# Performance work log

Hardware: AMD Instinct MI355X
Metric: run time of the kernel (lower is better)

The kernel has to match this reference:

```python
import jax
jax.config.update("jax_enable_x64", True)
import jax.numpy as jnp
import numpy as np

# NTT-friendly stand-in prime for BLS12-377 Fr (residues fit in int64, products in 62 bits)
P = 2013265921          # 15 * 2^27 + 1
GEN = 31                # generator of (Z/P)^*
COSET = 7               # coset shift generator
LOG_DOMAIN = 21
DOMAIN = 1 << LOG_DOMAIN
BATCH = 8


def _pow_table(base, length):
    """numpy int64 table [base^0, ..., base^(length-1)] mod P, built by doubling."""
    t = np.ones(length, dtype=np.int64)
    k = 1
    while k < length:
        mult = pow(int(base), k, P)          # exact python-int exponentiation
        end = min(2 * k, length)
        t[k:end] = (t[:end - k] * mult) % P  # < 2^62, no overflow
        k = end
    return t


def _bitrev(n):
    b = int(n).bit_length() - 1
    idx = np.arange(n, dtype=np.int64)
    rev = np.zeros(n, dtype=np.int64)
    for i in range(b):
        rev |= ((idx >> i) & 1) << (b - 1 - i)
    return rev


def _ntt_core(x, inverse):
    """Iterative radix-2 Cooley-Tukey NTT over rows of x: [batch, n] int64 residues mod P."""
    b, n = x.shape
    logn = n.bit_length() - 1
    root = pow(GEN, (P - 1) // n, P)         # primitive n-th root of unity
    if inverse:
        root = pow(root, P - 2, P)
    wpow = _pow_table(root, n // 2)          # root^j, j < n/2 (host-side, exact)
    x = x[:, jnp.asarray(_bitrev(n))]        # bit-reversal permutation
    for s in range(1, logn + 1):             # structural loop over log2(n) stages
        m = 1 << s
        half = m >> 1
        tw = jnp.asarray(wpow[:: n // m][:half])   # stage twiddles root^{j*n/m}
        xr = x.reshape(b, n // m, m)
        e, o = xr[..., :half], xr[..., half:]
        t = (o * tw) % P                     # butterfly: vectorized over all groups
        x = jnp.concatenate([(e + t) % P, (e - t) % P], axis=-1).reshape(b, n)
    return x


def setup_inputs() -> dict:
    key = jax.random.key(0)
    inp = jax.random.randint(key, (BATCH, DOMAIN), 0, P, dtype=jnp.int64)
    return {"input": inp, "is_intt": 0, "is_coset": 0}


def reference(input, is_intt, is_coset):
    x = jnp.mod(input, P)
    n = x.shape[-1]
    if (not is_intt) and is_coset:
        # coset NTT: multiply element i by COSET^i before the forward transform
        x = (x * jnp.asarray(_pow_table(COSET, n))) % P
    x = _ntt_core(x, inverse=bool(is_intt))
    if is_intt:
        if is_coset:
            # coset INTT: undo the coset shift after the inverse transform
            x = (x * jnp.asarray(_pow_table(pow(COSET, P - 2, P), n))) % P
        n_inv = pow(int(n), P - 2, P)
        x = (x * n_inv) % P                  # scale by n^{-1}
    return x
```

## Files before the change

kernel.cpp:

```cpp
#include <hip/hip_runtime.h>
#include <stdint.h>

typedef unsigned int u32;
typedef unsigned long long u64;

#define MOD_P 2013265921u

#define T_A      0
#define T_B      16384
#define T_W128P  32768
#define T_RP     49152
#define T_CLP    49216
#define T_CHP    65600
#define T_NINV   65728

__device__ __forceinline__ u32 mul64mod(u32 a, u32 b){ return (u32)((u64)a * b % MOD_P); }

__device__ u32 powmod(u32 b, u32 e){
  u32 r = 1;
  while (e){ if (e & 1) r = mul64mod(r, b); b = mul64mod(b, b); e >>= 1; }
  return r;
}

__device__ __forceinline__ u32 shoup_of(u32 v){ return (u32)(((u64)v << 32) / MOD_P); }

__device__ __forceinline__ u32 redP(u32 a){
  u32 b = a - MOD_P;
  return b < a ? b : a;
}

__device__ __forceinline__ u32 mul_shoup(u32 a, uint2 t){
  u32 q = __umulhi(a, t.y);
  u32 r = a * t.x - q * MOD_P;
  return redP(r);
}

__device__ __forceinline__ constexpr int rev4(int m){
  return ((m&1)<<3) | ((m&2)<<1) | ((m&4)>>1) | ((m&8)>>3);
}

__device__ __forceinline__ void bf(u32 &x, u32 &y, uint2 t){
  u32 s = redP(x + y);
  u32 d = x - y + MOD_P;
  x = s; y = mul_shoup(d, t);
}
__device__ __forceinline__ void bf0(u32 &x, u32 &y){
  u32 s = redP(x + y);
  u32 d = x - y + MOD_P;
  x = s; y = d;
}

__device__ __forceinline__ void stages_p1(u32 v[16], int b, const uint2* __restrict__ twl){
  #pragma unroll
  for (int m = 0; m < 8; ++m) bf(v[m], v[m+8], twl[b + 8*m]);
  #pragma unroll
  for (int g = 0; g < 2; ++g)
    #pragma unroll
    for (int m = 0; m < 4; ++m) bf(v[g*8+m], v[g*8+m+4], twl[(b + 8*m) << 1]);
  #pragma unroll
  for (int g = 0; g < 4; ++g)
    #pragma unroll
    for (int m = 0; m < 2; ++m) bf(v[g*4+m], v[g*4+m+2], twl[(b + 8*m) << 2]);
  #pragma unroll
  for (int k = 0; k < 8; ++k) bf(v[2*k], v[2*k+1], twl[b << 3]);
}
__device__ __forceinline__ void stages_p2(u32 v[16], const uint2* __restrict__ twl){
  #pragma unroll
  for (int g = 0; g < 2; ++g)
    #pragma unroll
    for (int m = 0; m < 4; ++m) bf(v[g*8+m], v[g*8+m+4], twl[m << 4]);
  #pragma unroll
  for (int g = 0; g < 4; ++g)
    #pragma unroll
    for (int m = 0; m < 2; ++m) bf(v[g*4+m], v[g*4+m+2], twl[m << 5]);
  #pragma unroll
  for (int k = 0; k < 8; ++k) bf0(v[2*k], v[2*k+1]);
}

__device__ __forceinline__ int cidx(int row, int a){
  return (row << 7) | (a ^ (row >> 2));
}

extern "C" __global__ void k_gen(uint2* __restrict__ tw, const int* __restrict__ f_intt){
  const u32 tid = blockIdx.x * 256 + threadIdx.x;
  const int intt = f_intt[0];
  const u32 MASK = (1u << 21) - 1;
  u32 v; int dst;
  if (tid < 16384){
    u32 e = (tid >> 7) * (tid & 127);
    if (intt) e = ((1u<<21) - e) & MASK;
    v = powmod(31u, 960u * e); dst = T_A + tid;
  } else if (tid < 32768){
    u32 i = tid - 16384;
    u32 e = (((i >> 7) * (i & 127)) << 7) & MASK;
    if (intt) e = ((1u<<21) - e) & MASK;
    v = powmod(31u, 960u * e); dst = T_B + i;
  } else if (tid < 49152){
    u32 i = tid - 32768;
    u32 e = (i << 7) & MASK;
    if (intt) e = ((1u<<21) - e) & MASK;
    v = powmod(31u, 960u * e); dst = T_W128P + i;
  } else if (tid < 65536){
    u32 i = tid - 49152;
    v = intt ? powmod(7u, (MOD_P - 1 - i) % (MOD_P - 1)) : powmod(7u, i);
    dst = T_CLP + i;
  } else if (tid < 65664){
    u32 e = (tid - 65536) << 14;
    v = intt ? powmod(7u, MOD_P - 1 - e) : powmod(7u, e);
    dst = T_CHP + (tid - 65536);
  } else if (tid < 65728){
    u32 e = ((tid - 65664) << 14) & MASK;
    if (intt) e = ((1u<<21) - e) & MASK;
    v = powmod(31u, 960u * e); dst = T_RP + (tid - 65664);
  } else if (tid == 65728){
    v = powmod(1u << 21, MOD_P - 2); dst = T_NINV;
  } else return;
  tw[dst] = make_uint2(v, shoup_of(v));
}

extern "C" __global__ void __launch_bounds__(1024, 8) k_passA_z(
    const u32* __restrict__ x, u32* __restrict__ z, const uint2* __restrict__ tw,
    const int* __restrict__ f_intt, const int* __restrict__ f_coset)
{
  __shared__ u32 lds[16384];
  const int wg = blockIdx.x;
  const int jb = wg & 127;
  const int batch = wg >> 7;
  const int t = threadIdx.x;
  const u32* xb = x + ((size_t)batch << 21) + (jb << 7);
  u32* zb = z + ((size_t)batch << 21) + (jb << 14);
  const uint2* twl = tw + T_RP;
  {
    const int q = t & 31, rr = t >> 5;
    uint4 tmp[4];
    #pragma unroll
    for (int i = 0; i < 4; ++i)
      tmp[i] = *(const uint4*)(xb + ((size_t)(rr + 32*i) << 14) + (q << 2));
    #pragma unroll
    for (int i = 0; i < 4; ++i){
      u32* d = &lds[((rr + 32*i) << 7) | (q << 2)];
      d[0] = redP(tmp[i].x); d[1] = redP(tmp[i].y);
      d[2] = redP(tmp[i].z); d[3] = redP(tmp[i].w);
    }
  }
  __syncthreads();
  const int jc = t & 127;
  const int b = __builtin_amdgcn_readfirstlane(t >> 7);
  u32 v[16];
  #pragma unroll
  for (int m = 0; m < 16; ++m) v[m] = lds[((b + 8*m) << 7) | jc];
  if ((f_intt[0] == 0) && (f_coset[0] != 0)){
    uint2 cl = tw[T_CLP + (jb << 7) + jc];
    #pragma unroll
    for (int m = 0; m < 16; ++m){
      v[m] = mul_shoup(v[m], cl);
      v[m] = mul_shoup(v[m], tw[T_CHP + b + 8*m]);
    }
  }
  stages_p1(v, b, twl);
  #pragma unroll
  for (int m = 0; m < 16; ++m) lds[((b + 8*m) << 7) | jc] = v[m];
  __syncthreads();
  #pragma unroll
  for (int m = 0; m < 16; ++m) v[m] = lds[((16*b + m) << 7) | jc];
  stages_p2(v, twl);
  const int rb = ((b&1)<<2) | (b&2) | ((b&4)>>2);
  #pragma unroll
  for (int m = 0; m < 16; ++m){
    const int ka = (rev4(m) << 3) | rb;
    u32 vv = mul_shoup(v[m], tw[T_A + (ka << 7) + jc]);
    vv = mul_shoup(vv, tw[T_W128P + ka * jb]);
    zb[(ka << 7) + jc] = vv;
  }
}

extern "C" __global__ void __launch_bounds__(1024, 8) k_passB_z(
    const u32* __restrict__ z, u32* __restrict__ y, const uint2* __restrict__ tw)
{
  __shared__ u32 lds[16384];
  const int wg = blockIdx.x;
  const int ka = wg & 127;
  const int batch = wg >> 7;
  const int t = threadIdx.x;
  const u32* zb = z + ((size_t)batch << 21) + (ka << 7);
  u32* yb = y + ((size_t)batch << 21) + ((size_t)ka << 14);
  const uint2* twl = tw + T_RP;
  {
    const int q = t & 31, rr = t >> 5;
    uint4 tmp[4];
    #pragma unroll
    for (int i = 0; i < 4; ++i)
      tmp[i] = *(const uint4*)(zb + ((size_t)(rr + 32*i) << 14) + (q << 2));
    #pragma unroll
    for (int i = 0; i < 4; ++i){
      u32* d = &lds[((rr + 32*i) << 7) | (q << 2)];
      d[0] = tmp[i].x; d[1] = tmp[i].y; d[2] = tmp[i].z; d[3] = tmp[i].w;
    }
  }
  __syncthreads();
  const int jc = t & 127;
  const int b = __builtin_amdgcn_readfirstlane(t >> 7);
  u32 v[16];
  #pragma unroll
  for (int m = 0; m < 16; ++m) v[m] = lds[((b + 8*m) << 7) | jc];
  stages_p1(v, b, twl);
  #pragma unroll
  for (int m = 0; m < 16; ++m) lds[((b + 8*m) << 7) | jc] = v[m];
  __syncthreads();
  #pragma unroll
  for (int m = 0; m < 16; ++m) v[m] = lds[((16*b + m) << 7) | jc];
  stages_p2(v, twl);
  const int rb = ((b&1)<<2) | (b&2) | ((b&4)>>2);
  #pragma unroll
  for (int m = 0; m < 16; ++m){
    const int kb = (rev4(m) << 3) | rb;
    u32 vv = mul_shoup(v[m], tw[T_B + (kb << 7) + jc]);
    yb[(kb << 7) + jc] = vv;
  }
}

extern "C" __global__ void __launch_bounds__(1024, 8) k_passA(
    const u32* __restrict__ x, u32* __restrict__ y, const uint2* __restrict__ tw,
    const int* __restrict__ f_intt, const int* __restrict__ f_coset)
{
  __shared__ u32 lds[16384];
  const int wg = blockIdx.x;
  const int jb = wg & 127;
  const int batch = wg >> 7;
  const int t = threadIdx.x;
  const u32* xb = x + ((size_t)batch << 21) + (jb << 7);
  u32* yb = y + ((size_t)batch << 21);
  const uint2* twl = tw + T_RP;
  {
    const int q = t & 31, rr = t >> 5;
    uint4 tmp[4];
    #pragma unroll
    for (int i = 0; i < 4; ++i)
      tmp[i] = *(const uint4*)(xb + ((size_t)(rr + 32*i) << 14) + (q << 2));
    #pragma unroll
    for (int i = 0; i < 4; ++i){
      u32* d = &lds[((rr + 32*i) << 7) | (q << 2)];
      d[0] = redP(tmp[i].x); d[1] = redP(tmp[i].y);
      d[2] = redP(tmp[i].z); d[3] = redP(tmp[i].w);
    }
  }
  __syncthreads();
  const int jc = t & 127;
  const int b = __builtin_amdgcn_readfirstlane(t >> 7);
  u32 v[16];
  #pragma unroll
  for (int m = 0; m < 16; ++m) v[m] = lds[((b + 8*m) << 7) | jc];
  if ((f_intt[0] == 0) && (f_coset[0] != 0)){
    uint2 cl = tw[T_CLP + (jb << 7) + jc];
    #pragma unroll
    for (int m = 0; m < 16; ++m){
      v[m] = mul_shoup(v[m], cl);
      v[m] = mul_shoup(v[m], tw[T_CHP + b + 8*m]);
    }
  }
  stages_p1(v, b, twl);
  #pragma unroll
  for (int m = 0; m < 16; ++m) lds[((b + 8*m) << 7) | jc] = v[m];
  __syncthreads();
  #pragma unroll
  for (int m = 0; m < 16; ++m) v[m] = lds[((16*b + m) << 7) | jc];
  stages_p2(v, twl);
  const int rb = ((b&1)<<2) | (b&2) | ((b&4)>>2);
  #pragma unroll
  for (int m = 0; m < 16; ++m){
    const int ka = (rev4(m) << 3) | rb;
    u32 vv = mul_shoup(v[m], tw[T_A + (ka << 7) + jc]);
    vv = mul_shoup(vv, tw[T_W128P + ka * jb]);
    yb[((size_t)ka << 14) + (jb << 7) + jc] = vv;
  }
}

extern "C" __global__ void __launch_bounds__(1024, 8) k_passB(
    u32* __restrict__ y, const uint2* __restrict__ tw)
{
  __shared__ u32 lds[16384];
  const int wg = blockIdx.x;
  const int ka = wg & 127;
  const int batch = wg >> 7;
  const int t = threadIdx.x;
  u32* yb = y + ((size_t)batch << 21) + ((size_t)ka << 14);
  const uint2* twl = tw + T_RP;
  {
    const uint4* s4 = (const uint4*)yb;
    uint4* l4 = (uint4*)lds;
    #pragma unroll
    for (int i = 0; i < 4; ++i) l4[t + 1024*i] = s4[t + 1024*i];
  }
  __syncthreads();
  const int jc = t & 127;
  const int b = __builtin_amdgcn_readfirstlane(t >> 7);
  u32 v[16];
  #pragma unroll
  for (int m = 0; m < 16; ++m) v[m] = lds[((b + 8*m) << 7) | jc];
  stages_p1(v, b, twl);
  #pragma unroll
  for (int m = 0; m < 16; ++m) lds[((b + 8*m) << 7) | jc] = v[m];
  __syncthreads();
  #pragma unroll
  for (int m = 0; m < 16; ++m) v[m] = lds[((16*b + m) << 7) | jc];
  stages_p2(v, twl);
  const int rb = ((b&1)<<2) | (b&2) | ((b&4)>>2);
  #pragma unroll
  for (int m = 0; m < 16; ++m){
    const int kb = (rev4(m) << 3) | rb;
    u32 vv = mul_shoup(v[m], tw[T_B + (kb << 7) + jc]);
    yb[(kb << 7) + jc] = vv;
  }
}

extern "C" __global__ void __launch_bounds__(1024, 8) k_passC(
    u32* __restrict__ y, const uint2* __restrict__ tw,
    const int* __restrict__ f_intt, const int* __restrict__ f_coset)
{
  __shared__ u32 lds[16384];
  const int wg = blockIdx.x;
  const int kb = wg & 127;
  const int batch = wg >> 7;
  u32* yb = y + ((size_t)batch << 21);
  const u32* base = yb + (kb << 7);
  const int t = threadIdx.x;
  {
    const int q = t & 31;
    const int rr = t >> 5;
    uint4 tmp[4];
    #pragma unroll
    for (int i = 0; i < 4; ++i)
      tmp[i] = *(const uint4*)(base + ((size_t)(rr + 32*i) << 14) + (q << 2));
    #pragma unroll
    for (int i = 0; i < 4; ++i){
      int kaL = rr + 32*i;
      lds[cidx(4*q+0, kaL)] = tmp[i].x;
      lds[cidx(4*q+1, kaL)] = tmp[i].y;
      lds[cidx(4*q+2, kaL)] = tmp[i].z;
      lds[cidx(4*q+3, kaL)] = tmp[i].w;
    }
  }
  __syncthreads();
  const int a = t & 127;
  const int b = __builtin_amdgcn_readfirstlane(t >> 7);
  const uint2* twl = tw + T_RP;
  u32 v[16];
  #pragma unroll
  for (int m = 0; m < 16; ++m) v[m] = lds[cidx(b + 8*m, a)];
  stages_p1(v, b, twl);
  #pragma unroll
  for (int m = 0; m < 16; ++m) lds[cidx(b + 8*m, a)] = v[m];
  __syncthreads();
  #pragma unroll
  for (int m = 0; m < 16; ++m) v[m] = lds[cidx(16*b + m, a)];
  stages_p2(v, twl);
  const int rb = ((b&1)<<2) | (b&2) | ((b&4)>>2);
  const int intt = f_intt[0];
  const int coset = f_coset[0];
  #pragma unroll
  for (int m = 0; m < 16; ++m){
    const int kc = (rev4(m) << 3) | rb;
    u32 vv = v[m];
    if (intt){
      vv = mul_shoup(vv, tw[T_NINV]);
      if (coset){
        vv = mul_shoup(vv, tw[T_CLP + (kb << 7) + a]);
        vv = mul_shoup(vv, tw[T_CHP + kc]);
      }
    } else {
      vv = redP(vv);
    }
    __builtin_nontemporal_store(vv, yb + ((size_t)kc << 14) + (kb << 7) + a);
  }
}

extern "C" void kernel_launch(void* const* d_in, const int* in_sizes, int n_in,
                              void* d_out, int out_size, void* d_ws, size_t ws_size,
                              hipStream_t stream)
{
  const u32* x = (const u32*)d_in[0];
  const int* f_intt  = (const int*)d_in[1];
  const int* f_coset = (const int*)d_in[2];
  u32* y   = (u32*)d_out;
  uint2* tw = (uint2*)d_ws;
  const int batch = in_sizes[0] >> 21;
  const int nwg = batch << 7;

  k_gen<<<257, 256, 0, stream>>>(tw, f_intt);

  const size_t zoff = (size_t)1 << 20;
  const size_t need = zoff + ((size_t)batch << 23);
  if (ws_size >= need){
    u32* z = (u32*)((char*)d_ws + zoff);
    k_passA_z<<<nwg, 1024, 0, stream>>>(x, z, tw, f_intt, f_coset);
    k_passB_z<<<nwg, 1024, 0, stream>>>(z, y, tw);
  } else {
    k_passA<<<nwg, 1024, 0, stream>>>(x, y, tw, f_intt, f_coset);
    k_passB<<<nwg, 1024, 0, stream>>>(y, tw);
  }
  k_passC<<<nwg, 1024, 0, stream>>>(y, tw, f_intt, f_coset);
}
```

Before: 99.73 us.

## Process two tiles per workgroup with prefetch of next tile during compute

Each of the three NTT passes now launches half as many workgroups, and each workgroup handles two tiles. The global loads for the second tile are issued before the first tile's butterflies and written to LDS midway, so their memory latency overlaps the first tile's compute. This adds barriers and register pressure for the prefetched data, and halves the grid to 512 workgroups, which may reduce occupancy and latency hiding across workgroups.

Result: slower. 138.4 us (+38.8%).

```diff
diff --git a/kernel.cpp b/kernel.cpp
--- a/kernel.cpp
+++ b/kernel.cpp
@@ -118,20 +118,22 @@
   tw[dst] = make_uint2(v, shoup_of(v));
 }
 
-extern "C" __global__ void __launch_bounds__(1024, 8) k_passA_z(
+extern "C" __global__ void __launch_bounds__(1024, 8) k_passA_p(
     const u32* __restrict__ x, u32* __restrict__ z, const uint2* __restrict__ tw,
-    const int* __restrict__ f_intt, const int* __restrict__ f_coset)
+    const int* __restrict__ f_intt, const int* __restrict__ f_coset, int H)
 {
   __shared__ u32 lds[16384];
-  const int wg = blockIdx.x;
-  const int jb = wg & 127;
-  const int batch = wg >> 7;
   const int t = threadIdx.x;
-  const u32* xb = x + ((size_t)batch << 21) + (jb << 7);
-  u32* zb = z + ((size_t)batch << 21) + (jb << 14);
+  const int q = t & 31, rr = t >> 5;
+  const int jc = t & 127;
+  const int b = __builtin_amdgcn_readfirstlane(t >> 7);
+  const int rb = ((b&1)<<2) | (b&2) | ((b&4)>>2);
   const uint2* twl = tw + T_RP;
+  const bool pre = (f_intt[0] == 0) && (f_coset[0] != 0);
+
+  int u = blockIdx.x;
   {
-    const int q = t & 31, rr = t >> 5;
+    const u32* xb = x + ((size_t)(u >> 7) << 21) + ((u & 127) << 7);
     uint4 tmp[4];
     #pragma unroll
     for (int i = 0; i < 4; ++i)
@@ -139,54 +141,74 @@
     #pragma unroll
     for (int i = 0; i < 4; ++i){
       u32* d = &lds[((rr + 32*i) << 7) | (q << 2)];
-      d[0] = redP(tmp[i].x); d[1] = redP(tmp[i].y);
-      d[2] = redP(tmp[i].z); d[3] = redP(tmp[i].w);
-    }
-  }
-  __syncthreads();
+      d[0]=redP(tmp[i].x); d[1]=redP(tmp[i].y); d[2]=redP(tmp[i].z); d[3]=redP(tmp[i].w);
+    }
+  }
+  __syncthreads();
+  #pragma unroll
+  for (int it = 0; it < 2; ++it){
+    uint4 tmp[4];
+    if (it == 0){
+      const int un = u + H;
+      const u32* xb = x + ((size_t)(un >> 7) << 21) + ((un & 127) << 7);
+      #pragma unroll
+      for (int i = 0; i < 4; ++i)
+        tmp[i] = *(const uint4*)(xb + ((size_t)(rr + 32*i) << 14) + (q << 2));
+    }
+    const int jb = u & 127;
+    u32* zb = z + ((size_t)(u >> 7) << 21) + (jb << 14);
+    u32 v[16];
+    #pragma unroll
+    for (int m = 0; m < 16; ++m) v[m] = lds[((b + 8*m) << 7) | jc];
+    if (pre){
+      uint2 cl = tw[T_CLP + (jb << 7) + jc];
+      #pragma unroll
+      for (int m = 0; m < 16; ++m){
+        v[m] = mul_shoup(v[m], cl);
+        v[m] = mul_shoup(v[m], tw[T_CHP + b + 8*m]);
+      }
+    }
+    stages_p1(v, b, twl);
+    #pragma unroll
+    for (int m = 0; m < 16; ++m) lds[((b + 8*m) << 7) | jc] = v[m];
+    __syncthreads();
+    #pragma unroll
+    for (int m = 0; m < 16; ++m) v[m] = lds[((16*b + m) << 7) | jc];
+    if (it == 0){
+      __syncthreads();
+      #pragma unroll
+      for (int i = 0; i < 4; ++i){
+        u32* d = &lds[((rr + 32*i) << 7) | (q << 2)];
+        d[0]=redP(tmp[i].x); d[1]=redP(tmp[i].y); d[2]=redP(tmp[i].z); d[3]=redP(tmp[i].w);
+      }
+    }
+    stages_p2(v, twl);
+    #pragma unroll
+    for (int m = 0; m < 16; ++m){
+      const int ka = (rev4(m) << 3) | rb;
+      u32 vv = mul_shoup(v[m], tw[T_A + (ka << 7) + jc]);
+      vv = mul_shoup(vv, tw[T_W128P + ka * jb]);
+      zb[(ka << 7) + jc] = vv;
+    }
+    if (it == 0) __syncthreads();
+    u += H;
+  }
+}
+
+extern "C" __global__ void __launch_bounds__(1024, 8) k_passB_p(
+    const u32* __restrict__ z, u32* __restrict__ y, const uint2* __restrict__ tw, int H)
+{
+  __shared__ u32 lds[16384];
+  const int t = threadIdx.x;
+  const int q = t & 31, rr = t >> 5;
   const int jc = t & 127;
   const int b = __builtin_amdgcn_readfirstlane(t >> 7);
-  u32 v[16];
-  #pragma unroll
-  for (int m = 0; m < 16; ++m) v[m] = lds[((b + 8*m) << 7) | jc];
-  if ((f_intt[0] == 0) && (f_coset[0] != 0)){
-    uint2 cl = tw[T_CLP + (jb << 7) + jc];
-    #pragma unroll
-    for (int m = 0; m < 16; ++m){
-      v[m] = mul_shoup(v[m], cl);
-      v[m] = mul_shoup(v[m], tw[T_CHP + b + 8*m]);
-    }
-  }
-  stages_p1(v, b, twl);
-  #pragma unroll
-  for (int m = 0; m < 16; ++m) lds[((b + 8*m) << 7) | jc] = v[m];
-  __syncthreads();
-  #pragma unroll
-  for (int m = 0; m < 16; ++m) v[m] = lds[((16*b + m) << 7) | jc];
-  stages_p2(v, twl);
   const int rb = ((b&1)<<2) | (b&2) | ((b&4)>>2);
-  #pragma unroll
-  for (int m = 0; m < 16; ++m){
-    const int ka = (rev4(m) << 3) | rb;
-    u32 vv = mul_shoup(v[m], tw[T_A + (ka << 7) + jc]);
-    vv = mul_shoup(vv, tw[T_W128P + ka * jb]);
-    zb[(ka << 7) + jc] = vv;
-  }
-}
-
-extern "C" __global__ void __launch_bounds__(1024, 8) k_passB_z(
-    const u32* __restrict__ z, u32* __restrict__ y, const uint2* __restrict__ tw)
-{
-  __shared__ u32 lds[16384];
-  const int wg = blockIdx.x;
-  const int ka = wg & 127;
-  const int batch = wg >> 7;
-  const int t = threadIdx.x;
-  const u32* zb = z + ((size_t)batch << 21) + (ka << 7);
-  u32* yb = y + ((size_t)batch << 21) + ((size_t)ka << 14);
   const uint2* twl = tw + T_RP;
+
+  int u = blockIdx.x;
   {
-    const int q = t & 31, rr = t >> 5;
+    const u32* zb = z + ((size_t)(u >> 7) << 21) + ((u & 127) << 7);
     uint4 tmp[4];
     #pragma unroll
     for (int i = 0; i < 4; ++i)
@@ -194,28 +216,132 @@
     #pragma unroll
     for (int i = 0; i < 4; ++i){
       u32* d = &lds[((rr + 32*i) << 7) | (q << 2)];
-      d[0] = tmp[i].x; d[1] = tmp[i].y; d[2] = tmp[i].z; d[3] = tmp[i].w;
-    }
-  }
-  __syncthreads();
-  const int jc = t & 127;
+      d[0]=tmp[i].x; d[1]=tmp[i].y; d[2]=tmp[i].z; d[3]=tmp[i].w;
+    }
+  }
+  __syncthreads();
+  #pragma unroll
+  for (int it = 0; it < 2; ++it){
+    uint4 tmp[4];
+    if (it == 0){
+      const int un = u + H;
+      const u32* zb = z + ((size_t)(un >> 7) << 21) + ((un & 127) << 7);
+      #pragma unroll
+      for (int i = 0; i < 4; ++i)
+        tmp[i] = *(const uint4*)(zb + ((size_t)(rr + 32*i) << 14) + (q << 2));
+    }
+    const int ka = u & 127;
+    u32* yb = y + ((size_t)(u >> 7) << 21) + ((size_t)ka << 14);
+    u32 v[16];
+    #pragma unroll
+    for (int m = 0; m < 16; ++m) v[m] = lds[((b + 8*m) << 7) | jc];
+    stages_p1(v, b, twl);
+    #pragma unroll
+    for (int m = 0; m < 16; ++m) lds[((b + 8*m) << 7) | jc] = v[m];
+    __syncthreads();
+    #pragma unroll
+    for (int m = 0; m < 16; ++m) v[m] = lds[((16*b + m) << 7) | jc];
+    if (it == 0){
+      __syncthreads();
+      #pragma unroll
+      for (int i = 0; i < 4; ++i){
+        u32* d = &lds[((rr + 32*i) << 7) | (q << 2)];
+        d[0]=tmp[i].x; d[1]=tmp[i].y; d[2]=tmp[i].z; d[3]=tmp[i].w;
+      }
+    }
+    stages_p2(v, twl);
+    #pragma unroll
+    for (int m = 0; m < 16; ++m){
+      const int kb = (rev4(m) << 3) | rb;
+      u32 vv = mul_shoup(v[m], tw[T_B + (kb << 7) + jc]);
+      yb[(kb << 7) + jc] = vv;
+    }
+    if (it == 0) __syncthreads();
+    u += H;
+  }
+}
+
+extern "C" __global__ void __launch_bounds__(1024, 8) k_passC_p(
+    u32* __restrict__ y, const uint2* __restrict__ tw,
+    const int* __restrict__ f_intt, const int* __restrict__ f_coset, int H)
+{
+  __shared__ u32 lds[16384];
+  const int t = threadIdx.x;
+  const int q = t & 31, rr = t >> 5;
+  const int a = t & 127;
   const int b = __builtin_amdgcn_readfirstlane(t >> 7);
-  u32 v[16];
-  #pragma unroll
-  for (int m = 0; m < 16; ++m) v[m] = lds[((b + 8*m) << 7) | jc];
-  stages_p1(v, b, twl);
-  #pragma unroll
-  for (int m = 0; m < 16; ++m) lds[((b + 8*m) << 7) | jc] = v[m];
-  __syncthreads();
-  #pragma unroll
-  for (int m = 0; m < 16; ++m) v[m] = lds[((16*b + m) << 7) | jc];
-  stages_p2(v, twl);
   const int rb = ((b&1)<<2) | (b&2) | ((b&4)>>2);
-  #pragma unroll
-  for (int m = 0; m < 16; ++m){
-    const int kb = (rev4(m) << 3) | rb;
-    u32 vv = mul_shoup(v[m], tw[T_B + (kb << 7) + jc]);
-    yb[(kb << 7) + jc] = vv;
+  const uint2* twl = tw + T_RP;
+  const int intt = f_intt[0];
+  const int coset = f_coset[0];
+
+  int u = blockIdx.x;
+  {
+    const u32* base = y + ((size_t)(u >> 7) << 21) + ((u & 127) << 7);
+    uint4 tmp[4];
+    #pragma unroll
+    for (int i = 0; i < 4; ++i)
+      tmp[i] = *(const uint4*)(base + ((size_t)(rr + 32*i) << 14) + (q << 2));
+    #pragma unroll
+    for (int i = 0; i < 4; ++i){
+      int kaL = rr + 32*i;
+      lds[cidx(4*q+0, kaL)] = tmp[i].x;
+      lds[cidx(4*q+1, kaL)] = tmp[i].y;
+      lds[cidx(4*q+2, kaL)] = tmp[i].z;
+      lds[cidx(4*q+3, kaL)] = tmp[i].w;
+    }
+  }
+  __syncthreads();
+  #pragma unroll
+  for (int it = 0; it < 2; ++it){
+    uint4 tmp[4];
+    if (it == 0){
+      const int un = u + H;
+      const u32* base = y + ((size_t)(un >> 7) << 21) + ((un & 127) << 7);
+      #pragma unroll
+      for (int i = 0; i < 4; ++i)
+        tmp[i] = *(const uint4*)(base + ((size_t)(rr + 32*i) << 14) + (q << 2));
+    }
+    const int kb = u & 127;
+    u32* yb = y + ((size_t)(u >> 7) << 21);
+    u32 v[16];
+    #pragma unroll
+    for (int m = 0; m < 16; ++m) v[m] = lds[cidx(b + 8*m, a)];
+    stages_p1(v, b, twl);
+    #pragma unroll
+    for (int m = 0; m < 16; ++m) lds[cidx(b + 8*m, a)] = v[m];
+    __syncthreads();
+    #pragma unroll
+    for (int m = 0; m < 16; ++m) v[m] = lds[cidx(16*b + m, a)];
+    if (it == 0){
+      __syncthreads();
+      #pragma unroll
+      for (int i = 0; i < 4; ++i){
+        int kaL = rr + 32*i;
+        lds[cidx(4*q+0, kaL)] = tmp[i].x;
+        lds[cidx(4*q+1, kaL)] = tmp[i].y;
+        lds[cidx(4*q+2, kaL)] = tmp[i].z;
+        lds[cidx(4*q+3, kaL)] = tmp[i].w;
+      }
+    }
+    stages_p2(v, twl);
+    #pragma unroll
+    for (int m = 0; m < 16; ++m){
+      const int kc = (rev4(m) << 3) | rb;
+      u32 vv = v[m];
+      if (intt){
+        vv = mul_shoup(vv, tw[T_NINV]);
+        if (coset){
+          vv = mul_shoup(vv, tw[T_CLP + (kb << 7) + a]);
+          vv = mul_shoup(vv, tw[T_CHP + kc]);
+        }
+      } else {
+        vv = redP(vv);
+      }
+      __builtin_nontemporal_store(vv, yb + ((size_t)kc << 14) + (kb << 7) + a);
+    }
+    if (it == 0) __syncthreads();
+    u += H;
   }
 }
 
@@ -384,19 +510,21 @@
   u32* y   = (u32*)d_out;
   uint2* tw = (uint2*)d_ws;
   const int batch = in_sizes[0] >> 21;
-  const int nwg = batch << 7;
+  const int nunits = batch << 7;
 
   k_gen<<<257, 256, 0, stream>>>(tw, f_intt);
 
   const size_t zoff = (size_t)1 << 20;
   const size_t need = zoff + ((size_t)batch << 23);
-  if (ws_size >= need){
+  if (ws_size >= need && (nunits & 1) == 0){
     u32* z = (u32*)((char*)d_ws + zoff);
-    k_passA_z<<<nwg, 1024, 0, stream>>>(x, z, tw, f_intt, f_coset);
-    k_passB_z<<<nwg, 1024, 0, stream>>>(z, y, tw);
+    const int H = nunits >> 1;
+    k_passA_p<<<H, 1024, 0, stream>>>(x, z, tw, f_intt, f_coset, H);
+    k_passB_p<<<H, 1024, 0, stream>>>(z, y, tw, H);
+    k_passC_p<<<H, 1024, 0, stream>>>(y, tw, f_intt, f_coset, H);
   } else {
-    k_passA<<<nwg, 1024, 0, stream>>>(x, y, tw, f_intt, f_coset);
-    k_passB<<<nwg, 1024, 0, stream>>>(y, tw);
-  }
-  k_passC<<<nwg, 1024, 0, stream>>>(y, tw, f_intt, f_coset);
-}
+    k_passA<<<nunits, 1024, 0, stream>>>(x, y, tw, f_intt, f_coset);
+    k_passB<<<nunits, 1024, 0, stream>>>(y, tw);
+    k_passC<<<nunits, 1024, 0, stream>>>(y, tw, f_intt, f_coset);
+  }
+}
```
